# Kernel tuning notes

Hardware: AMD Instinct MI355X
Metric: run time of the kernel (lower is better)

Reference implementation:

```python
import math
import jax, jax.numpy as jnp
import numpy as np

B, T, E = 2, 2048, 2048
NUM_HEADS = 16
H = NUM_HEADS // 2          # differential head pairs = 8
D = E // NUM_HEADS          # head_dim = 128
DEPTH = 12
LAMBDA_INIT = 0.8 - 0.6 * math.exp(-0.3 * DEPTH)
EPS = 1e-5


def setup_inputs() -> dict:
    key = jax.random.key(0)
    ks = jax.random.split(key, 10)
    sc = lambda k, shape, std: jax.random.normal(k, shape, dtype=jnp.float32) * std
    return {
        "x": jax.random.normal(ks[0], (B, T, E), dtype=jnp.float32),
        "Wq": sc(ks[1], (E, E), 0.02),   # [in, out]
        "Wk": sc(ks[2], (E, E), 0.02),   # n_rep == 1 -> k/v proj width = embed_dim
        "Wv": sc(ks[3], (E, E), 0.02),
        "Wo": sc(ks[4], (E, E), 0.02),
        "lambda_q1": sc(ks[5], (D,), 0.1),
        "lambda_k1": sc(ks[6], (D,), 0.1),
        "lambda_q2": sc(ks[7], (D,), 0.1),
        "lambda_k2": sc(ks[8], (D,), 0.1),
        "g": jnp.ones((2 * D,), dtype=jnp.float32),  # RMSNorm weight
    }


def _forward(x, Wq, Wk, Wv, Wo, lq1, lk1, lq2, lk2, g):
    Bz, Tl, _ = x.shape
    # projections; view(bsz, T, 2*H, D).reshape(bsz, T, H, 2, D): adjacent head
    # pairs become the two differential components.
    q = (x @ Wq).reshape(Bz, Tl, H, 2, D)
    k = (x @ Wk).reshape(Bz, Tl, H, 2, D)
    v = (x @ Wv).reshape(Bz, Tl, H, 2 * D)   # value width is 2*head_dim

    scale = D ** -0.5                         # SDPA default scaling
    causal = jnp.tril(jnp.ones((Tl, Tl), dtype=bool))  # is_causal=True

    def attend(qc, kc):
        # qc, kc: [B, T, H, D]
        s = jnp.einsum('bthd,bshd->bhts', qc, kc) * scale
        s = jnp.where(causal, s, -jnp.inf)
        a = jax.nn.softmax(s, axis=-1)
        return jnp.einsum('bhts,bshe->bthe', a, v)  # [B, T, H, 2D]

    # interleaved q/k + repeated v in the single SDPA == two attention maps on full V
    o1 = attend(q[..., 0, :], k[..., 0, :])
    o2 = attend(q[..., 1, :], k[..., 1, :])

    lam = jnp.exp(jnp.sum(lq1 * lk1)) - jnp.exp(jnp.sum(lq2 * lk2)) + LAMBDA_INIT
    o = o1 - lam * o2
    # RMSNorm over last dim (2*head_dim), eps=1e-5, learned weight g
    o = o * jax.lax.rsqrt(jnp.mean(o * o, axis=-1, keepdims=True) + EPS) * g
    o = o * (1.0 - LAMBDA_INIT)
    return o.reshape(Bz, Tl, E) @ Wo


def reference(x, Wq, Wk, Wv, Wo, lambda_q1, lambda_k1, lambda_q2, lambda_k2, g):
    return _forward(x, Wq, Wk, Wv, Wo, lambda_q1, lambda_k1, lambda_q2, lambda_k2, g)
```

## Files before the change

### kernel.cpp

```cpp
#include <hip/hip_runtime.h>
#include <stdint.h>
#include <math.h>


typedef unsigned short u16;
typedef short bf16x8 __attribute__((ext_vector_type(8)));
typedef float f32x4 __attribute__((ext_vector_type(4)));

typedef uint32_t __attribute__((address_space(1))) as1_u32;
typedef uint32_t __attribute__((address_space(3))) as3_u32;

#define LAMBDA_INIT 0.78360576653162453f

__device__ __forceinline__ u16 f2bf(float f) {
  uint32_t u = __float_as_uint(f);
  u += 0x7FFFu + ((u >> 16) & 1u);
  return (u16)(u >> 16);
}
__device__ __forceinline__ float bf2f(u16 v) {
  return __uint_as_float(((uint32_t)v) << 16);
}

__device__ __forceinline__ void async16(u16* lds, const u16* g) {
  __builtin_amdgcn_global_load_lds((const as1_u32*)(uintptr_t)g,
                                   (as3_u32*)(uint32_t)(uintptr_t)lds, 16, 0, 0);
}

__device__ __forceinline__ f32x4 mfma16(bf16x8 a, bf16x8 b, f32x4 c) {
  return __builtin_amdgcn_mfma_f32_16x16x32_bf16(a, b, c, 0, 0, 0);
}


__global__ void cast_x_kernel(const float* __restrict__ x, u16* __restrict__ xb, int n4) {
  int i = blockIdx.x * 256 + threadIdx.x;
  if (i < n4) {
    float4 v = ((const float4*)x)[i];
    ushort4 o;
    o.x = f2bf(v.x); o.y = f2bf(v.y); o.z = f2bf(v.z); o.w = f2bf(v.w);
    ((ushort4*)xb)[i] = o;
  }
}

__global__ void transpose_w_kernel(const float* __restrict__ W, u16* __restrict__ Wt) {
  __shared__ float tile[32][33];
  int tx = threadIdx.x, ty = threadIdx.y;
  int c0 = blockIdx.x * 32, r0 = blockIdx.y * 32;
#pragma unroll
  for (int i = 0; i < 32; i += 8)
    tile[ty + i][tx] = W[(size_t)(r0 + ty + i) * 2048 + c0 + tx];
  __syncthreads();
#pragma unroll
  for (int i = 0; i < 32; i += 8)
    Wt[(size_t)(c0 + ty + i) * 2048 + r0 + tx] = f2bf(tile[tx][ty + i]);
}

__global__ void lam_kernel(const float* __restrict__ lq1, const float* __restrict__ lk1,
                           const float* __restrict__ lq2, const float* __restrict__ lk2,
                           float* __restrict__ out) {
  int L = threadIdx.x;
  float d1 = lq1[L] * lk1[L] + lq1[L + 64] * lk1[L + 64];
  float d2 = lq2[L] * lk2[L] + lq2[L + 64] * lk2[L + 64];
#pragma unroll
  for (int m = 1; m < 64; m <<= 1) {
    d1 += __shfl_xor(d1, m);
    d2 += __shfl_xor(d2, m);
  }
  if (L == 0) out[0] = __expf(d1) - __expf(d2) + LAMBDA_INIT;
}

template <int OUT_BF16>
__global__ __launch_bounds__(256, 2) void gemm_bt_kernel(const u16* __restrict__ A,
                                                         const u16* __restrict__ Bt,
                                                         void* __restrict__ Cout,
                                                         int M, int N, int K) {
  __shared__ __attribute__((aligned(16))) u16 As[128 * 32];
  __shared__ __attribute__((aligned(16))) u16 Bs[128 * 32];
  int t = threadIdx.x;
  int lane = t & 63, w = t >> 6;
  int lr = lane & 15, lq = lane >> 4;
  int m0 = blockIdx.y * 128, n0 = blockIdx.x * 128;
  int wm = (w >> 1) * 64, wn = (w & 1) * 64;
  const u16* Ab = A + (size_t)m0 * K;
  const u16* Bb = Bt + (size_t)n0 * K;
  f32x4 acc[4][4] = {};
  int r0 = t >> 2;
  int kc0 = (t & 3) * 8;

  for (int k0 = 0; k0 < K; k0 += 32) {
    __syncthreads();
    async16(&As[t * 8], Ab + (size_t)r0 * K + k0 + kc0);
    async16(&Bs[t * 8], Bb + (size_t)r0 * K + k0 + kc0);
    async16(&As[(256 + t) * 8], Ab + (size_t)(64 + r0) * K + k0 + kc0);
    async16(&Bs[(256 + t) * 8], Bb + (size_t)(64 + r0) * K + k0 + kc0);
    __syncthreads();
    bf16x8 a[4], b[4];
#pragma unroll
    for (int mi = 0; mi < 4; mi++)
      a[mi] = *(const bf16x8*)&As[(wm + mi * 16 + lr) * 32 + lq * 8];
#pragma unroll
    for (int ni = 0; ni < 4; ni++)
      b[ni] = *(const bf16x8*)&Bs[(wn + ni * 16 + lr) * 32 + lq * 8];
#pragma unroll
    for (int mi = 0; mi < 4; mi++)
#pragma unroll
      for (int ni = 0; ni < 4; ni++)
        acc[mi][ni] = mfma16(a[mi], b[ni], acc[mi][ni]);
  }
#pragma unroll
  for (int mi = 0; mi < 4; mi++) {
#pragma unroll
    for (int ni = 0; ni < 4; ni++) {
#pragma unroll
      for (int r = 0; r < 4; r++) {
        int row = m0 + wm + mi * 16 + lq * 4 + r;
        int col = n0 + wn + ni * 16 + lr;
        if (OUT_BF16)
          ((u16*)Cout)[(size_t)row * N + col] = f2bf(acc[mi][ni][r]);
        else
          ((float*)Cout)[(size_t)row * N + col] = acc[mi][ni][r];
      }
    }
  }
}


struct FlashCtx {
  const u16* Qbase;
  const u16* Kbase;
  const u16* Vbase;
  int t, w, lr, lq;
};

__device__ __forceinline__ void stage_k(const FlashCtx& cx, int jc, u16* Kn) {
#pragma unroll
  for (int i = 0; i < 4; i++) {
    int q = cx.t + i * 256;
    int row = q >> 4, gp = q & 15;
    int gg = (gp & 8) | ((gp & 7) ^ (row & 7));
    async16(&Kn[q * 8], cx.Kbase + (size_t)(jc + row) * 4096 + gg * 8);
  }
}

__device__ __forceinline__ void stage_v(const FlashCtx& cx, int jc, u16* Vs) {
#pragma unroll
  for (int i = 0; i < 8; i++) {
    int q = cx.t + i * 256;
    int e = q >> 3, gp = q & 7;
    int gg = gp ^ (e & 7);
    async16(&Vs[q * 8], cx.Vbase + (size_t)e * 4096 + jc + gg * 8);
  }
}

__global__ __launch_bounds__(256, 2) void flash_diff_kernel(const u16* __restrict__ QKb,
                                                            const u16* __restrict__ Vt,
                                                            u16* __restrict__ o12b) {
  __shared__ __attribute__((aligned(16))) u16 Ks0[64 * 128];
  __shared__ __attribute__((aligned(16))) u16 Ks1[64 * 128];
  __shared__ __attribute__((aligned(16))) u16 Vs[256 * 64];
  __shared__ __attribute__((aligned(16))) u16 Ps[4][16 * 88];

  int t = threadIdx.x;
  FlashCtx cx;
  cx.t = t; cx.w = t >> 6;
  cx.lr = t & 15; cx.lq = (t >> 4) & 3;

  int idx = blockIdx.x;
  int xcd = idx & 7, slot = idx >> 3;
  int pairI = slot & 15, ghi = slot >> 4;
  int g = ghi * 8 + xcd;
  int bh = g >> 1, c = g & 1;
  int b = bh >> 3, h = bh & 7;

  cx.Qbase = QKb + (size_t)b * 2048 * 4096 + h * 256 + c * 128;
  cx.Kbase = cx.Qbase + 2048;
  cx.Vbase = Vt + (size_t)(h * 256) * 4096 + b * 2048;
  u16* Op = o12b + (size_t)c * (4096ull * 2048) + (size_t)b * 2048 * 2048 + h * 256;
  u16* PsW = Ps[cx.w];

  u16* Kc = Ks0;
  u16* Kn = Ks1;

  stage_k(cx, 0, Kc);

#pragma unroll 1
  for (int phase = 0; phase < 2; phase++) {
    int qi = phase ? (31 - pairI) : pairI;
    int q0 = qi * 64;
    int nst = qi + 1;

    bf16x8 qa[4];
#pragma unroll
    for (int ks = 0; ks < 4; ks++)
      qa[ks] = *(const bf16x8*)&cx.Qbase[(size_t)(q0 + cx.w * 16 + cx.lr) * 4096 +
                                         ks * 32 + cx.lq * 8];

    f32x4 acc[16] = {};
    f32x4 lacc = {};
    float m_ = -INFINITY;
    int rowmax = q0 + cx.w * 16 + 15;

#pragma unroll 1
    for (int j = 0; j < nst; j++) {
      int jc = j * 64;
      int njc = (j + 1 < nst) ? (j + 1) * 64 : (phase == 0 ? 0 : -1);

      __syncthreads();
      if (njc >= 0) stage_k(cx, njc, Kn);
      stage_v(cx, jc, Vs);

      bool act = (jc <= rowmax);
      if (act) {
        f32x4 sacc[4] = {};
#pragma unroll
        for (int ks = 0; ks < 4; ks++) {
#pragma unroll
          for (int ni = 0; ni < 4; ni++) {
            int row = ni * 16 + cx.lr;
            int gk = ks * 4 + cx.lq;
            int gp = (gk & 8) | ((gk & 7) ^ (row & 7));
            bf16x8 kb = *(const bf16x8*)&Kc[row * 128 + gp * 8];
            sacc[ni] = mfma16(qa[ks], kb, sacc[ni]);
          }
        }

        const float k2 = 0.12753257550036097f;
        float s2[4][4];
        bool diag = (jc + 63 > q0 + cx.w * 16);
#pragma unroll
        for (int ni = 0; ni < 4; ni++)
#pragma unroll
          for (int r = 0; r < 4; r++) {
            float v = sacc[ni][r] * k2;
            if (diag) {
              int colg = jc + ni * 16 + cx.lr;
              int rowg = q0 + cx.w * 16 + cx.lq * 4 + r;
              if (colg > rowg) v = -INFINITY;
            }
            s2[ni][r] = v;
          }

        float sm = fmaxf(
            fmaxf(fmaxf(fmaxf(s2[0][0], s2[0][1]), fmaxf(s2[0][2], s2[0][3])),
                  fmaxf(fmaxf(s2[1][0], s2[1][1]), fmaxf(s2[1][2], s2[1][3]))),
            fmaxf(fmaxf(fmaxf(s2[2][0], s2[2][1]), fmaxf(s2[2][2], s2[2][3])),
                  fmaxf(fmaxf(s2[3][0], s2[3][1]), fmaxf(s2[3][2], s2[3][3]))));
        float mo = m_;
        if (__any(sm > mo + 8.0f)) {
          float mv = sm;
          mv = fmaxf(mv, __shfl_xor(mv, 1));
          mv = fmaxf(mv, __shfl_xor(mv, 2));
          mv = fmaxf(mv, __shfl_xor(mv, 4));
          mv = fmaxf(mv, __shfl_xor(mv, 8));
          mv = fmaxf(mv, __shfl_xor(mv, 16));
          mv = fmaxf(mv, __shfl_xor(mv, 32));
          float mn = fmaxf(mo, mv);
          float a = __builtin_amdgcn_exp2f(mo - mn);
#pragma unroll
          for (int ei = 0; ei < 16; ei++)
#pragma unroll
            for (int r = 0; r < 4; r++) acc[ei][r] *= a;
#pragma unroll
          for (int r = 0; r < 4; r++) lacc[r] *= a;
          m_ = mn;
          mo = mn;
        }

#pragma unroll
        for (int ni = 0; ni < 4; ni++)
#pragma unroll
          for (int r = 0; r < 4; r++) {
            float p = __builtin_amdgcn_exp2f(s2[ni][r] - mo);
            PsW[(cx.lq * 4 + r) * 88 + ni * 16 + cx.lr] =
                (u16)(__float_as_uint(p) >> 16);
          }
      }

      __syncthreads();
      if (act) {
        const bf16x8 onesb = {0x3F80, 0x3F80, 0x3F80, 0x3F80,
                              0x3F80, 0x3F80, 0x3F80, 0x3F80};
        bf16x8 pa0 = *(const bf16x8*)&PsW[cx.lr * 88 + cx.lq * 8];
        bf16x8 pa1 = *(const bf16x8*)&PsW[cx.lr * 88 + 32 + cx.lq * 8];
#pragma unroll
        for (int ei = 0; ei < 16; ei++) {
          int e = ei * 16 + cx.lr;
          int g0 = cx.lq ^ (e & 7);
          int g1 = g0 ^ 4;
          bf16x8 vb0 = *(const bf16x8*)&Vs[e * 64 + g0 * 8];
          bf16x8 vb1 = *(const bf16x8*)&Vs[e * 64 + g1 * 8];
          acc[ei] = mfma16(pa0, vb0, acc[ei]);
          acc[ei] = mfma16(pa1, vb1, acc[ei]);
        }
        lacc = mfma16(pa0, onesb, lacc);
        lacc = mfma16(pa1, onesb, lacc);
      }

      u16* tmp = Kc; Kc = Kn; Kn = tmp;
    }

#pragma unroll
    for (int r = 0; r < 4; r++) {
      float inv = 1.0f / lacc[r];
      int row = q0 + cx.w * 16 + cx.lq * 4 + r;
#pragma unroll
      for (int ei = 0; ei < 16; ei++)
        Op[(size_t)row * 2048 + ei * 16 + cx.lr] = f2bf(acc[ei][r] * inv);
    }
  }
}

__global__ void combine_kernel(const u16* __restrict__ o12b, const float* __restrict__ lamp,
                               const float* __restrict__ g, u16* __restrict__ ob) {
  __shared__ float red[4];
  int t = threadIdx.x;
  int grp = blockIdx.x;
  size_t idx = (size_t)grp * 256 + t;
  const size_t comp = 4096ull * 2048;
  float lam = lamp[0];
  float v = bf2f(o12b[idx]) - lam * bf2f(o12b[idx + comp]);
  float ss = v * v;
  ss += __shfl_xor(ss, 1);
  ss += __shfl_xor(ss, 2);
  ss += __shfl_xor(ss, 4);
  ss += __shfl_xor(ss, 8);
  ss += __shfl_xor(ss, 16);
  ss += __shfl_xor(ss, 32);
  if ((t & 63) == 0) red[t >> 6] = ss;
  __syncthreads();
  float tot = red[0] + red[1] + red[2] + red[3];
  float scale = rsqrtf(tot * (1.0f / 256.0f) + 1e-5f) * (1.0f - LAMBDA_INIT);
  ob[(size_t)(grp >> 3) * 2048 + (grp & 7) * 256 + t] = f2bf(v * scale * g[t]);
}


extern "C" void kernel_launch(void* const* d_in, const int* in_sizes, int n_in,
                              void* d_out, int out_size, void* d_ws, size_t ws_size,
                              hipStream_t stream) {
  const float* x   = (const float*)d_in[0];
  const float* Wq  = (const float*)d_in[1];
  const float* Wk  = (const float*)d_in[2];
  const float* Wv  = (const float*)d_in[3];
  const float* Wo  = (const float*)d_in[4];
  const float* lq1 = (const float*)d_in[5];
  const float* lk1 = (const float*)d_in[6];
  const float* lq2 = (const float*)d_in[7];
  const float* lk2 = (const float*)d_in[8];
  const float* g   = (const float*)d_in[9];

  char* ws = (char*)d_ws;
  u16* xb    = (u16*)(ws);
  u16* Wtq   = (u16*)(ws + 16777216);
  u16* Wtk   = (u16*)(ws + 25165824);
  u16* Wtv   = (u16*)(ws + 33554432);
  u16* Wto   = (u16*)(ws + 41943040);
  u16* QKb   = (u16*)(ws + 50331648);
  u16* Vt    = (u16*)(ws + 83886080);
  u16* o12b  = (u16*)(ws + 100663296);
  u16* ob    = (u16*)(ws + 134217728);
  float* lamp = (float*)(ws + 150994944);

  cast_x_kernel<<<8192, 256, 0, stream>>>(x, xb, 2097152);
  dim3 tb(32, 8), tg(64, 64);
  transpose_w_kernel<<<tg, tb, 0, stream>>>(Wq, Wtq);
  transpose_w_kernel<<<tg, tb, 0, stream>>>(Wk, Wtk);
  transpose_w_kernel<<<tg, tb, 0, stream>>>(Wv, Wtv);
  transpose_w_kernel<<<tg, tb, 0, stream>>>(Wo, Wto);
  lam_kernel<<<1, 64, 0, stream>>>(lq1, lk1, lq2, lk2, lamp);

  gemm_bt_kernel<1><<<dim3(32, 32), 256, 0, stream>>>(xb, Wtq, QKb, 4096, 4096, 2048);
  gemm_bt_kernel<1><<<dim3(32, 16), 256, 0, stream>>>(Wtv, xb, Vt, 2048, 4096, 2048);

  flash_diff_kernel<<<512, 256, 0, stream>>>(QKb, Vt, o12b);
  combine_kernel<<<32768, 256, 0, stream>>>(o12b, lamp, g, ob);
  gemm_bt_kernel<0><<<dim3(16, 32), 256, 0, stream>>>(ob, Wto, (float*)d_out, 4096, 2048, 2048);
}
```

Before: 433.0 us.

## Restructure flash kernel with direct V register loads and deferred PV pipelining

The flash attention kernel drops the LDS staging of V. Each wave now loads its own V fragments straight from global memory into registers, and the PV product for the previous tile is deferred so it overlaps with the current QK and softmax, using double-buffered P tiles and per-wave rescale factors kept in shared memory. Waves now split the output dimension instead of query rows, and the row sums are exchanged through LDS at the end. Separately, the four weight transposes are merged into one launch and launch bounds are raised to 3 blocks per CU, which risks register spills and adds more global V traffic.

After: 491.0 us. +13.4%, slower.

```diff
diff --git a/kernel.cpp b/kernel.cpp
--- a/kernel.cpp
+++ b/kernel.cpp
@@ -41,8 +41,13 @@
   }
 }
 
-__global__ void transpose_w_kernel(const float* __restrict__ W, u16* __restrict__ Wt) {
+__global__ void transpose_w4_kernel(const float* __restrict__ W0, const float* __restrict__ W1,
+                                    const float* __restrict__ W2, const float* __restrict__ W3,
+                                    u16* __restrict__ Wt4) {
   __shared__ float tile[32][33];
+  int z = blockIdx.z;
+  const float* W = (z == 0) ? W0 : (z == 1) ? W1 : (z == 2) ? W2 : W3;
+  u16* Wt = Wt4 + (size_t)z * 4194304;
   int tx = threadIdx.x, ty = threadIdx.y;
   int c0 = blockIdx.x * 32, r0 = blockIdx.y * 32;
 #pragma unroll
@@ -69,7 +74,7 @@
 }
 
 template <int OUT_BF16>
-__global__ __launch_bounds__(256, 2) void gemm_bt_kernel(const u16* __restrict__ A,
+__global__ __launch_bounds__(256, 3) void gemm_bt_kernel(const u16* __restrict__ A,
                                                          const u16* __restrict__ Bt,
                                                          void* __restrict__ Cout,
                                                          int M, int N, int K) {
@@ -141,28 +146,55 @@
   }
 }
 
-__device__ __forceinline__ void stage_v(const FlashCtx& cx, int jc, u16* Vs) {
-#pragma unroll
-  for (int i = 0; i < 8; i++) {
-    int q = cx.t + i * 256;
-    int e = q >> 3, gp = q & 7;
-    int gg = gp ^ (e & 7);
-    async16(&Vs[q * 8], cx.Vbase + (size_t)e * 4096 + jc + gg * 8);
-  }
-}
-
-__global__ __launch_bounds__(256, 2) void flash_diff_kernel(const u16* __restrict__ QKb,
+__device__ __forceinline__ void load_v(const u16* Vw, int jp, bf16x8 (&vfr)[4][2]) {
+#pragma unroll
+  for (int ei = 0; ei < 4; ei++)
+#pragma unroll
+    for (int hh = 0; hh < 2; hh++)
+      vfr[ei][hh] = *(const bf16x8*)(Vw + (size_t)ei * 16 * 4096 + jp + hh * 32);
+}
+
+__device__ __forceinline__ void pv_apply(f32x4 (&acc)[4][4], const bf16x8 (&vfr)[4][2],
+                                         const u16* Pr, const float* abp, int lr, int lq) {
+  float am[4];
+  am[0] = abp[0]; am[1] = abp[1]; am[2] = abp[2]; am[3] = abp[3];
+  if (am[0] != 1.0f || am[1] != 1.0f || am[2] != 1.0f || am[3] != 1.0f) {
+#pragma unroll
+    for (int mi = 0; mi < 4; mi++)
+#pragma unroll
+      for (int ei = 0; ei < 4; ei++)
+#pragma unroll
+        for (int r = 0; r < 4; r++) acc[mi][ei][r] *= am[mi];
+  }
+  __builtin_amdgcn_s_setprio(1);
+#pragma unroll
+  for (int mi = 0; mi < 4; mi++) {
+    bf16x8 pa0 = *(const bf16x8*)&Pr[(mi * 16 + lr) * 72 + lq * 8];
+    bf16x8 pa1 = *(const bf16x8*)&Pr[(mi * 16 + lr) * 72 + 32 + lq * 8];
+#pragma unroll
+    for (int ei = 0; ei < 4; ei++) {
+      acc[mi][ei] = mfma16(pa0, vfr[ei][0], acc[mi][ei]);
+      acc[mi][ei] = mfma16(pa1, vfr[ei][1], acc[mi][ei]);
+    }
+  }
+  __builtin_amdgcn_s_setprio(0);
+}
+
+__global__ __launch_bounds__(256, 3) void flash_diff_kernel(const u16* __restrict__ QKb,
                                                             const u16* __restrict__ Vt,
                                                             u16* __restrict__ o12b) {
   __shared__ __attribute__((aligned(16))) u16 Ks0[64 * 128];
   __shared__ __attribute__((aligned(16))) u16 Ks1[64 * 128];
-  __shared__ __attribute__((aligned(16))) u16 Vs[256 * 64];
-  __shared__ __attribute__((aligned(16))) u16 Ps[4][16 * 88];
+  __shared__ __attribute__((aligned(16))) u16 Pb[2][64 * 72];
+  __shared__ float ab[2][4];
+  __shared__ float lf[64];
 
   int t = threadIdx.x;
   FlashCtx cx;
   cx.t = t; cx.w = t >> 6;
   cx.lr = t & 15; cx.lq = (t >> 4) & 3;
+  int lr = cx.lr, lq = cx.lq, w = cx.w;
+  int lane = t & 63;
 
   int idx = blockIdx.x;
   int xcd = idx & 7, slot = idx >> 3;
@@ -175,12 +207,17 @@
   cx.Kbase = cx.Qbase + 2048;
   cx.Vbase = Vt + (size_t)(h * 256) * 4096 + b * 2048;
   u16* Op = o12b + (size_t)c * (4096ull * 2048) + (size_t)b * 2048 * 2048 + h * 256;
-  u16* PsW = Ps[cx.w];
+
+  const u16* Vw = cx.Vbase + (size_t)(w * 64 + lr) * 4096 + lq * 8;
 
   u16* Kc = Ks0;
   u16* Kn = Ks1;
-
   stage_k(cx, 0, Kc);
+  __syncthreads();
+
+  const float k2 = 0.12753257550036097f;
+  const bf16x8 onesb = {0x3F80, 0x3F80, 0x3F80, 0x3F80,
+                        0x3F80, 0x3F80, 0x3F80, 0x3F80};
 
 #pragma unroll 1
   for (int phase = 0; phase < 2; phase++) {
@@ -191,121 +228,120 @@
     bf16x8 qa[4];
 #pragma unroll
     for (int ks = 0; ks < 4; ks++)
-      qa[ks] = *(const bf16x8*)&cx.Qbase[(size_t)(q0 + cx.w * 16 + cx.lr) * 4096 +
-                                         ks * 32 + cx.lq * 8];
-
-    f32x4 acc[16] = {};
+      qa[ks] = *(const bf16x8*)&cx.Qbase[(size_t)(q0 + w * 16 + lr) * 4096 +
+                                         ks * 32 + lq * 8];
+
+    f32x4 acc[4][4] = {};
     f32x4 lacc = {};
     float m_ = -INFINITY;
-    int rowmax = q0 + cx.w * 16 + 15;
 
 #pragma unroll 1
     for (int j = 0; j < nst; j++) {
       int jc = j * 64;
-      int njc = (j + 1 < nst) ? (j + 1) * 64 : (phase == 0 ? 0 : -1);
-
+
+      bf16x8 vfr[4][2];
+      if (j > 0) load_v(Vw, jc - 64, vfr);
+
+      bool stg = (j + 1 < nst) || (phase == 0 && j == nst - 1);
+      if (stg) stage_k(cx, (j + 1 < nst) ? jc + 64 : 0, Kn);
+
+      f32x4 sacc[4] = {};
+#pragma unroll
+      for (int ks = 0; ks < 4; ks++) {
+#pragma unroll
+        for (int ni = 0; ni < 4; ni++) {
+          int row = ni * 16 + lr;
+          int gk = ks * 4 + lq;
+          int gp = (gk & 8) | ((gk & 7) ^ (row & 7));
+          bf16x8 kb = *(const bf16x8*)&Kc[row * 128 + gp * 8];
+          sacc[ni] = mfma16(qa[ks], kb, sacc[ni]);
+        }
+      }
+
+      float s2[4][4];
+      bool diag = (jc + 63 > q0 + w * 16);
+#pragma unroll
+      for (int ni = 0; ni < 4; ni++)
+#pragma unroll
+        for (int r = 0; r < 4; r++) {
+          float v = sacc[ni][r] * k2;
+          if (diag) {
+            int colg = jc + ni * 16 + lr;
+            int rowg = q0 + w * 16 + lq * 4 + r;
+            if (colg > rowg) v = -INFINITY;
+          }
+          s2[ni][r] = v;
+        }
+
+      float sm = fmaxf(
+          fmaxf(fmaxf(fmaxf(s2[0][0], s2[0][1]), fmaxf(s2[0][2], s2[0][3])),
+                fmaxf(fmaxf(s2[1][0], s2[1][1]), fmaxf(s2[1][2], s2[1][3]))),
+          fmaxf(fmaxf(fmaxf(s2[2][0], s2[2][1]), fmaxf(s2[2][2], s2[2][3])),
+                fmaxf(fmaxf(s2[3][0], s2[3][1]), fmaxf(s2[3][2], s2[3][3]))));
+      float mo = m_;
+      float aw = 1.0f;
+      if (__any(sm > mo + 8.0f)) {
+        float mv = sm;
+        mv = fmaxf(mv, __shfl_xor(mv, 1));
+        mv = fmaxf(mv, __shfl_xor(mv, 2));
+        mv = fmaxf(mv, __shfl_xor(mv, 4));
+        mv = fmaxf(mv, __shfl_xor(mv, 8));
+        mv = fmaxf(mv, __shfl_xor(mv, 16));
+        mv = fmaxf(mv, __shfl_xor(mv, 32));
+        float mn = fmaxf(mo, mv);
+        aw = __builtin_amdgcn_exp2f(mo - mn);
+        m_ = mn;
+        mo = mn;
+#pragma unroll
+        for (int r = 0; r < 4; r++) lacc[r] *= aw;
+      }
+
+      u16* Pw = Pb[j & 1];
+#pragma unroll
+      for (int ni = 0; ni < 4; ni++)
+#pragma unroll
+        for (int r = 0; r < 4; r++) {
+          float p = __builtin_amdgcn_exp2f(s2[ni][r] - mo);
+          Pw[(w * 16 + lq * 4 + r) * 72 + ni * 16 + lr] =
+              (u16)(__float_as_uint(p) >> 16);
+        }
+      if (lane == 0) ab[j & 1][w] = aw;
+
+      bf16x8 po0 = *(const bf16x8*)&Pw[(w * 16 + lr) * 72 + lq * 8];
+      bf16x8 po1 = *(const bf16x8*)&Pw[(w * 16 + lr) * 72 + 32 + lq * 8];
+      lacc = mfma16(po0, onesb, lacc);
+      lacc = mfma16(po1, onesb, lacc);
+
+      if (j > 0) pv_apply(acc, vfr, Pb[(j - 1) & 1], &ab[(j - 1) & 1][0], lr, lq);
+
+      if (stg) { u16* tmp = Kc; Kc = Kn; Kn = tmp; }
       __syncthreads();
-      if (njc >= 0) stage_k(cx, njc, Kn);
-      stage_v(cx, jc, Vs);
-
-      bool act = (jc <= rowmax);
-      if (act) {
-        f32x4 sacc[4] = {};
-#pragma unroll
-        for (int ks = 0; ks < 4; ks++) {
-#pragma unroll
-          for (int ni = 0; ni < 4; ni++) {
-            int row = ni * 16 + cx.lr;
-            int gk = ks * 4 + cx.lq;
-            int gp = (gk & 8) | ((gk & 7) ^ (row & 7));
-            bf16x8 kb = *(const bf16x8*)&Kc[row * 128 + gp * 8];
-            sacc[ni] = mfma16(qa[ks], kb, sacc[ni]);
-          }
-        }
-
-        const float k2 = 0.12753257550036097f;
-        float s2[4][4];
-        bool diag = (jc + 63 > q0 + cx.w * 16);
-#pragma unroll
-        for (int ni = 0; ni < 4; ni++)
-#pragma unroll
-          for (int r = 0; r < 4; r++) {
-            float v = sacc[ni][r] * k2;
-            if (diag) {
-              int colg = jc + ni * 16 + cx.lr;
-              int rowg = q0 + cx.w * 16 + cx.lq * 4 + r;
-              if (colg > rowg) v = -INFINITY;
-            }
-            s2[ni][r] = v;
-          }
-
-        float sm = fmaxf(
-            fmaxf(fmaxf(fmaxf(s2[0][0], s2[0][1]), fmaxf(s2[0][2], s2[0][3])),
-                  fmaxf(fmaxf(s2[1][0], s2[1][1]), fmaxf(s2[1][2], s2[1][3]))),
-            fmaxf(fmaxf(fmaxf(s2[2][0], s2[2][1]), fmaxf(s2[2][2], s2[2][3])),
-                  fmaxf(fmaxf(s2[3][0], s2[3][1]), fmaxf(s2[3][2], s2[3][3]))));
-        float mo = m_;
-        if (__any(sm > mo + 8.0f)) {
-          float mv = sm;
-          mv = fmaxf(mv, __shfl_xor(mv, 1));
-          mv = fmaxf(mv, __shfl_xor(mv, 2));
-          mv = fmaxf(mv, __shfl_xor(mv, 4));
-          mv = fmaxf(mv, __shfl_xor(mv, 8));
-          mv = fmaxf(mv, __shfl_xor(mv, 16));
-          mv = fmaxf(mv, __shfl_xor(mv, 32));
-          float mn = fmaxf(mo, mv);
-          float a = __builtin_amdgcn_exp2f(mo - mn);
-#pragma unroll
-          for (int ei = 0; ei < 16; ei++)
-#pragma unroll
-            for (int r = 0; r < 4; r++) acc[ei][r] *= a;
-#pragma unroll
-          for (int r = 0; r < 4; r++) lacc[r] *= a;
-          m_ = mn;
-          mo = mn;
-        }
-
-#pragma unroll
-        for (int ni = 0; ni < 4; ni++)
-#pragma unroll
-          for (int r = 0; r < 4; r++) {
-            float p = __builtin_amdgcn_exp2f(s2[ni][r] - mo);
-            PsW[(cx.lq * 4 + r) * 88 + ni * 16 + cx.lr] =
-                (u16)(__float_as_uint(p) >> 16);
-          }
+    }
+
+    {
+      bf16x8 vfr[4][2];
+      load_v(Vw, (nst - 1) * 64, vfr);
+      pv_apply(acc, vfr, Pb[(nst - 1) & 1], &ab[(nst - 1) & 1][0], lr, lq);
+    }
+
+    if (lr == 0) {
+#pragma unroll
+      for (int r = 0; r < 4; r++) lf[w * 16 + lq * 4 + r] = lacc[r];
+    }
+    __syncthreads();
+#pragma unroll
+    for (int mi = 0; mi < 4; mi++) {
+#pragma unroll
+      for (int r = 0; r < 4; r++) {
+        float inv = 1.0f / lf[mi * 16 + lq * 4 + r];
+        int row = q0 + mi * 16 + lq * 4 + r;
+#pragma unroll
+        for (int ei = 0; ei < 4; ei++)
+          Op[(size_t)row * 2048 + w * 64 + ei * 16 + lr] =
+              f2bf(acc[mi][ei][r] * inv);
       }
-
-      __syncthreads();
-      if (act) {
-        const bf16x8 onesb = {0x3F80, 0x3F80, 0x3F80, 0x3F80,
-                              0x3F80, 0x3F80, 0x3F80, 0x3F80};
-        bf16x8 pa0 = *(const bf16x8*)&PsW[cx.lr * 88 + cx.lq * 8];
-        bf16x8 pa1 = *(const bf16x8*)&PsW[cx.lr * 88 + 32 + cx.lq * 8];
-#pragma unroll
-        for (int ei = 0; ei < 16; ei++) {
-          int e = ei * 16 + cx.lr;
-          int g0 = cx.lq ^ (e & 7);
-          int g1 = g0 ^ 4;
-          bf16x8 vb0 = *(const bf16x8*)&Vs[e * 64 + g0 * 8];
-          bf16x8 vb1 = *(const bf16x8*)&Vs[e * 64 + g1 * 8];
-          acc[ei] = mfma16(pa0, vb0, acc[ei]);
-          acc[ei] = mfma16(pa1, vb1, acc[ei]);
-        }
-        lacc = mfma16(pa0, onesb, lacc);
-        lacc = mfma16(pa1, onesb, lacc);
-      }
-
-      u16* tmp = Kc; Kc = Kn; Kn = tmp;
-    }
-
-#pragma unroll
-    for (int r = 0; r < 4; r++) {
-      float inv = 1.0f / lacc[r];
-      int row = q0 + cx.w * 16 + cx.lq * 4 + r;
-#pragma unroll
-      for (int ei = 0; ei < 16; ei++)
-        Op[(size_t)row * 2048 + ei * 16 + cx.lr] = f2bf(acc[ei][r] * inv);
-    }
+    }
+    __syncthreads();
   }
 }
 
@@ -350,7 +386,6 @@
   char* ws = (char*)d_ws;
   u16* xb    = (u16*)(ws);
   u16* Wtq   = (u16*)(ws + 16777216);
-  u16* Wtk   = (u16*)(ws + 25165824);
   u16* Wtv   = (u16*)(ws + 33554432);
   u16* Wto   = (u16*)(ws + 41943040);
   u16* QKb   = (u16*)(ws + 50331648);
@@ -360,11 +395,7 @@
   float* lamp = (float*)(ws + 150994944);
 
   cast_x_kernel<<<8192, 256, 0, stream>>>(x, xb, 2097152);
-  dim3 tb(32, 8), tg(64, 64);
-  transpose_w_kernel<<<tg, tb, 0, stream>>>(Wq, Wtq);
-  transpose_w_kernel<<<tg, tb, 0, stream>>>(Wk, Wtk);
-  transpose_w_kernel<<<tg, tb, 0, stream>>>(Wv, Wtv);
-  transpose_w_kernel<<<tg, tb, 0, stream>>>(Wo, Wto);
+  transpose_w4_kernel<<<dim3(64, 64, 4), dim3(32, 8), 0, stream>>>(Wq, Wk, Wv, Wo, Wtq);
   lam_kernel<<<1, 64, 0, stream>>>(lq1, lk1, lq2, lk2, lamp);
 
   gemm_bt_kernel<1><<<dim3(32, 32), 256, 0, stream>>>(xb, Wtq, QKb, 4096, 4096, 2048);
```

## Double GEMM k-tile with XOR-swizzled LDS, batch weight transposes, prioritize PV MFMAs

Applied to the files above, without the earlier changes.

The GEMM now stages 64-wide k tiles instead of 32, halving the number of barrier pairs per tile. LDS placement is XOR-swizzled so the wider rows are read without bank conflicts, and the occupancy hint rises from 2 to 3 blocks per CU. The four weight transposes are merged into one launch using blockIdx.z, relying on the Wq, Wk, Wv and Wo slots being contiguous in workspace. The attention PV MFMA section is wrapped in s_setprio to favour that wave's matrix issue; the larger LDS footprint may limit the requested occupancy.

After: 403.6 us. -6.8%, faster.

```diff
diff --git a/kernel.cpp b/kernel.cpp
--- a/kernel.cpp
+++ b/kernel.cpp
@@ -41,8 +41,13 @@
   }
 }
 
-__global__ void transpose_w_kernel(const float* __restrict__ W, u16* __restrict__ Wt) {
+__global__ void transpose_w4_kernel(const float* __restrict__ W0, const float* __restrict__ W1,
+                                    const float* __restrict__ W2, const float* __restrict__ W3,
+                                    u16* __restrict__ Wt4) {
   __shared__ float tile[32][33];
+  int z = blockIdx.z;
+  const float* W = (z == 0) ? W0 : (z == 1) ? W1 : (z == 2) ? W2 : W3;
+  u16* Wt = Wt4 + (size_t)z * 4194304;
   int tx = threadIdx.x, ty = threadIdx.y;
   int c0 = blockIdx.x * 32, r0 = blockIdx.y * 32;
 #pragma unroll
@@ -69,12 +74,12 @@
 }
 
 template <int OUT_BF16>
-__global__ __launch_bounds__(256, 2) void gemm_bt_kernel(const u16* __restrict__ A,
+__global__ __launch_bounds__(256, 3) void gemm_bt_kernel(const u16* __restrict__ A,
                                                          const u16* __restrict__ Bt,
                                                          void* __restrict__ Cout,
                                                          int M, int N, int K) {
-  __shared__ __attribute__((aligned(16))) u16 As[128 * 32];
-  __shared__ __attribute__((aligned(16))) u16 Bs[128 * 32];
+  __shared__ __attribute__((aligned(16))) u16 As[128 * 64];
+  __shared__ __attribute__((aligned(16))) u16 Bs[128 * 64];
   int t = threadIdx.x;
   int lane = t & 63, w = t >> 6;
   int lr = lane & 15, lq = lane >> 4;
@@ -83,28 +88,34 @@
   const u16* Ab = A + (size_t)m0 * K;
   const u16* Bb = Bt + (size_t)n0 * K;
   f32x4 acc[4][4] = {};
-  int r0 = t >> 2;
-  int kc0 = (t & 3) * 8;
-
-  for (int k0 = 0; k0 < K; k0 += 32) {
+
+  for (int k0 = 0; k0 < K; k0 += 64) {
     __syncthreads();
-    async16(&As[t * 8], Ab + (size_t)r0 * K + k0 + kc0);
-    async16(&Bs[t * 8], Bb + (size_t)r0 * K + k0 + kc0);
-    async16(&As[(256 + t) * 8], Ab + (size_t)(64 + r0) * K + k0 + kc0);
-    async16(&Bs[(256 + t) * 8], Bb + (size_t)(64 + r0) * K + k0 + kc0);
+#pragma unroll
+    for (int i = 0; i < 4; i++) {
+      int q = t + i * 256;
+      int row = q >> 3, gp = q & 7;
+      int gg = gp ^ (row & 7);
+      async16(&As[q * 8], Ab + (size_t)row * K + k0 + gg * 8);
+      async16(&Bs[q * 8], Bb + (size_t)row * K + k0 + gg * 8);
+    }
     __syncthreads();
-    bf16x8 a[4], b[4];
-#pragma unroll
-    for (int mi = 0; mi < 4; mi++)
-      a[mi] = *(const bf16x8*)&As[(wm + mi * 16 + lr) * 32 + lq * 8];
-#pragma unroll
-    for (int ni = 0; ni < 4; ni++)
-      b[ni] = *(const bf16x8*)&Bs[(wn + ni * 16 + lr) * 32 + lq * 8];
-#pragma unroll
-    for (int mi = 0; mi < 4; mi++)
-#pragma unroll
-      for (int ni = 0; ni < 4; ni++)
-        acc[mi][ni] = mfma16(a[mi], b[ni], acc[mi][ni]);
+#pragma unroll
+    for (int kk = 0; kk < 2; kk++) {
+      bf16x8 a[4], b[4];
+#pragma unroll
+      for (int mi = 0; mi < 4; mi++) {
+        int ra = wm + mi * 16 + lr;
+        int rb = wn + mi * 16 + lr;
+        a[mi] = *(const bf16x8*)&As[ra * 64 + ((kk * 4 + lq) ^ (ra & 7)) * 8];
+        b[mi] = *(const bf16x8*)&Bs[rb * 64 + ((kk * 4 + lq) ^ (rb & 7)) * 8];
+      }
+#pragma unroll
+      for (int mi = 0; mi < 4; mi++)
+#pragma unroll
+        for (int ni = 0; ni < 4; ni++)
+          acc[mi][ni] = mfma16(a[mi], b[ni], acc[mi][ni]);
+    }
   }
 #pragma unroll
   for (int mi = 0; mi < 4; mi++) {
@@ -281,6 +292,7 @@
                               0x3F80, 0x3F80, 0x3F80, 0x3F80};
         bf16x8 pa0 = *(const bf16x8*)&PsW[cx.lr * 88 + cx.lq * 8];
         bf16x8 pa1 = *(const bf16x8*)&PsW[cx.lr * 88 + 32 + cx.lq * 8];
+        __builtin_amdgcn_s_setprio(1);
 #pragma unroll
         for (int ei = 0; ei < 16; ei++) {
           int e = ei * 16 + cx.lr;
@@ -293,6 +305,7 @@
         }
         lacc = mfma16(pa0, onesb, lacc);
         lacc = mfma16(pa1, onesb, lacc);
+        __builtin_amdgcn_s_setprio(0);
       }
 
       u16* tmp = Kc; Kc = Kn; Kn = tmp;
@@ -350,7 +363,6 @@
   char* ws = (char*)d_ws;
   u16* xb    = (u16*)(ws);
   u16* Wtq   = (u16*)(ws + 16777216);
-  u16* Wtk   = (u16*)(ws + 25165824);
   u16* Wtv   = (u16*)(ws + 33554432);
   u16* Wto   = (u16*)(ws + 41943040);
   u16* QKb   = (u16*)(ws + 50331648);
@@ -360,11 +372,7 @@
   float* lamp = (float*)(ws + 150994944);
 
   cast_x_kernel<<<8192, 256, 0, stream>>>(x, xb, 2097152);
-  dim3 tb(32, 8), tg(64, 64);
-  transpose_w_kernel<<<tg, tb, 0, stream>>>(Wq, Wtq);
-  transpose_w_kernel<<<tg, tb, 0, stream>>>(Wk, Wtk);
-  transpose_w_kernel<<<tg, tb, 0, stream>>>(Wv, Wtv);
-  transpose_w_kernel<<<tg, tb, 0, stream>>>(Wo, Wto);
+  transpose_w4_kernel<<<dim3(64, 64, 4), dim3(32, 8), 0, stream>>>(Wq, Wk, Wv, Wo, Wtq);
   lam_kernel<<<1, 64, 0, stream>>>(lq1, lk1, lq2, lk2, lamp);
 
   gemm_bt_kernel<1><<<dim3(32, 32), 256, 0, stream>>>(xb, Wtq, QKb, 4096, 4096, 2048);
```
